# Performance work log

Measured on AMD Instinct MI355X. Metric: run time of the kernel, lower is better.

The kernel has to match this reference:

```python
import jax, jax.numpy as jnp
import numpy as np

D_MODEL = 2560
NUM_HEADS = 32
NUM_KV_HEADS = 8
HEAD_DIM = 128
ROPE_THETA = 5e6
EPS = 1e-6
G = NUM_KV_HEADS
Q_PER_KV = NUM_HEADS // NUM_KV_HEADS


def setup_inputs() -> dict:
    key = jax.random.key(0)
    ks = jax.random.split(key, 5)
    B, S = 1, 2048
    scale = 0.02
    return {
        "x": jax.random.normal(ks[0], (B, S, D_MODEL), jnp.float32),
        "Wq": jax.random.normal(ks[1], (NUM_HEADS * HEAD_DIM, D_MODEL), jnp.float32) * scale,
        "Wk": jax.random.normal(ks[2], (NUM_KV_HEADS * HEAD_DIM, D_MODEL), jnp.float32) * scale,
        "Wv": jax.random.normal(ks[3], (NUM_KV_HEADS * HEAD_DIM, D_MODEL), jnp.float32) * scale,
        "Wo": jax.random.normal(ks[4], (D_MODEL, NUM_HEADS * HEAD_DIM), jnp.float32) * scale,
        "q_norm_w": jnp.ones((HEAD_DIM,), jnp.float32),
        "k_norm_w": jnp.ones((HEAD_DIM,), jnp.float32),
    }


def _rms_norm(x, w):
    var = jnp.mean(jnp.square(x), axis=-1, keepdims=True)
    return x * jax.lax.rsqrt(var + EPS) * w


def _rope(x, pos):
    # x: (b, h, s, d); HF-style rotate_half RoPE
    d = x.shape[-1]
    inv_freq = 1.0 / (ROPE_THETA ** (jnp.arange(0, d, 2, dtype=jnp.float32) / d))
    ang = pos[:, None].astype(jnp.float32) * inv_freq[None, :]      # (s, d/2)
    cos = jnp.concatenate([jnp.cos(ang), jnp.cos(ang)], axis=-1)     # (s, d)
    sin = jnp.concatenate([jnp.sin(ang), jnp.sin(ang)], axis=-1)
    x1, x2 = x[..., : d // 2], x[..., d // 2 :]
    rot = jnp.concatenate([-x2, x1], axis=-1)
    return x * cos + rot * sin


def reference(x, Wq, Wk, Wv, Wo, q_norm_w, k_norm_w):
    B, S, _ = x.shape
    pos = jnp.arange(S)
    q = (x @ Wq.T).reshape(B, S, NUM_HEADS, HEAD_DIM).transpose(0, 2, 1, 3)
    k = (x @ Wk.T).reshape(B, S, NUM_KV_HEADS, HEAD_DIM).transpose(0, 2, 1, 3)
    v = (x @ Wv.T).reshape(B, S, NUM_KV_HEADS, HEAD_DIM).transpose(0, 2, 1, 3)
    q = _rope(_rms_norm(q, q_norm_w), pos)
    k = _rope(_rms_norm(k, k_norm_w), pos)
    new_cache_k, new_cache_v = k, v
    # GQA: (b, g, h, s, d) against (b, g, k, d)
    qg = q.reshape(B, G, Q_PER_KV, S, HEAD_DIM)
    scores = jnp.einsum("bghsd,bgkd->bghsk", qg, k) / (HEAD_DIM ** 0.5)
    causal = jnp.triu(jnp.full((S, S), -jnp.inf, jnp.float32), k=1)
    scores = scores + causal
    attn = jax.nn.softmax(scores, axis=-1)
    out = jnp.einsum("bghsk,bgkd->bghsd", attn, v)
    out = out.reshape(B, NUM_HEADS, S, HEAD_DIM).transpose(0, 2, 1, 3).reshape(B, S, NUM_HEADS * HEAD_DIM)
    out = out @ Wo.T
    return (out, new_cache_k, new_cache_v)
```

## Files before the change

### kernel.cpp

```cpp
#include <hip/hip_runtime.h>
#include <hip/hip_bf16.h>
#include <math.h>

#define S_LEN  2048
#define DMODEL 2560
#define NHEADS 32
#define NKV    8
#define HD     128
#define QKDIM  (NHEADS * HD)
#define KVDIM  (NKV * HD)

typedef __bf16 bf16x8 __attribute__((ext_vector_type(8)));
typedef float  f32x4  __attribute__((ext_vector_type(4)));
typedef unsigned short u16;

#define AS1 __attribute__((address_space(1)))
#define AS3 __attribute__((address_space(3)))

__device__ __forceinline__ void load16_to_lds(const void* g, void* l) {
    __builtin_amdgcn_global_load_lds((const AS1 void*)g, (AS3 void*)l, 16, 0, 0);
}

__device__ __forceinline__ u16 f2bf(float f) {
    unsigned u = __builtin_bit_cast(unsigned, f);
    return (u16)((u + 0x7fff + ((u >> 16) & 1)) >> 16);
}

#define PHASE_BAR() do { __builtin_amdgcn_sched_barrier(0);            \
                         __builtin_amdgcn_s_barrier();                 \
                         __builtin_amdgcn_sched_barrier(0); } while (0)
#define WAIT_LGKM0() do { asm volatile("s_waitcnt lgkmcnt(0)" ::: "memory"); \
                          __builtin_amdgcn_sched_barrier(0); } while (0)

__device__ __forceinline__ const bf16x8* fragp(const __bf16* hbase, int row, int colb) {
    int b = (row << 7) | colb;
    b ^= ((b >> 9) & 1) << 5;
    return (const bf16x8*)((const char*)hbase + b);
}

__device__ __forceinline__ void stage_half(const __bf16* __restrict__ g0, int Kp,
                                           __bf16* l0, int wave, int lane) {
#pragma unroll
    for (int j = 0; j < 2; ++j) {
        const int p = ((wave * 2 + j) << 10) | (lane << 4);
        const int b = p ^ (((p >> 9) & 1) << 5);
        load16_to_lds((const char*)g0 + (size_t)(b >> 7) * (Kp * 2) + (b & 127),
                      (char*)l0 + ((wave * 2 + j) << 10));
    }
}

#define N4_X   (S_LEN * DMODEL / 4)
#define N4_WQ  (QKDIM * DMODEL / 4)
#define N4_WK  (KVDIM * DMODEL / 4)
#define N4_ALL (N4_X + N4_WQ + 2 * N4_WK)

__global__ __launch_bounds__(256) void convert_inputs(const float* __restrict__ x,
                                                      const float* __restrict__ wq,
                                                      const float* __restrict__ wk,
                                                      const float* __restrict__ wv,
                                                      u16* __restrict__ xb,
                                                      u16* __restrict__ wb) {
    const int stride = gridDim.x * 256;
    for (int i = blockIdx.x * 256 + threadIdx.x; i < N4_ALL; i += stride) {
        const float4* src;
        ushort4* dst;
        if (i < N4_X) {
            src = (const float4*)x + i;
            dst = (ushort4*)xb + i;
        } else {
            const int j = i - N4_X;
            dst = (ushort4*)wb + j;
            if (j < N4_WQ)                  src = (const float4*)wq + j;
            else if (j < N4_WQ + N4_WK)     src = (const float4*)wk + (j - N4_WQ);
            else                            src = (const float4*)wv + (j - N4_WQ - N4_WK);
        }
        float4 v = *src;
        ushort4 r;
        r.x = f2bf(v.x); r.y = f2bf(v.y); r.z = f2bf(v.z); r.w = f2bf(v.w);
        *dst = r;
    }
}

__global__ __launch_bounds__(256) void f32_to_bf16_k(const float* __restrict__ in,
                                                     u16* __restrict__ out, int n4) {
    int i = blockIdx.x * 256 + threadIdx.x;
    const int stride = gridDim.x * 256;
    for (; i < n4; i += stride) {
        float4 v = ((const float4*)in)[i];
        ushort4 r;
        r.x = f2bf(v.x); r.y = f2bf(v.y); r.z = f2bf(v.z); r.w = f2bf(v.w);
        ((ushort4*)out)[i] = r;
    }
}

__global__ __launch_bounds__(64) void rope_table(float* __restrict__ ct,
                                                 float* __restrict__ st) {
    const int s = blockIdx.x;
    const int i = threadIdx.x;
    const double invf = pow(5.0e6, -(double)i / 64.0);
    const double ang  = (double)s * invf;
    ct[s * 64 + i] = (float)cos(ang);
    st[s * 64 + i] = (float)sin(ang);
}

__global__ __launch_bounds__(256) void gemm_bf16_nt(const __bf16* __restrict__ A,
                                                    const __bf16* __restrict__ B,
                                                    float* __restrict__ C,
                                                    int M, int N, int K) {
    __shared__ __align__(16) __bf16 Als[128 * 64];
    __shared__ __align__(16) __bf16 Bls[128 * 64];
    const int tid  = threadIdx.x;
    const int lane = tid & 63;
    const int wave = tid >> 6;
    const int wm   = wave >> 1, wn = wave & 1;
    const int m0   = blockIdx.y * 128;
    const int n0   = blockIdx.x * 128;
    const int frow = lane & 15;
    const int fkq  = lane >> 4;

    f32x4 acc[4][4];
#pragma unroll
    for (int t = 0; t < 4; ++t)
#pragma unroll
        for (int u = 0; u < 4; ++u)
            acc[t][u] = (f32x4){0.f, 0.f, 0.f, 0.f};

    for (int k0 = 0; k0 < K; k0 += 64) {
        __syncthreads();
#pragma unroll
        for (int i = 0; i < 2; ++i) {
            const int mt  = i * 4 + wave;
            const int row = mt * 16 + frow;
#pragma unroll
            for (int kh = 0; kh < 2; ++kh) {
                const int col = k0 + kh * 32 + fkq * 8;
                load16_to_lds(A + (size_t)(m0 + row) * K + col,
                              &Als[(size_t)((mt * 2 + kh) * 64) * 8]);
                load16_to_lds(B + (size_t)(n0 + row) * K + col,
                              &Bls[(size_t)((mt * 2 + kh) * 64) * 8]);
            }
        }
        __syncthreads();

#pragma unroll
        for (int kh = 0; kh < 2; ++kh) {
            bf16x8 af[4], bfr[4];
#pragma unroll
            for (int t = 0; t < 4; ++t)
                af[t]  = *(const bf16x8*)&Als[(((wm * 4 + t) * 2 + kh) * 64 + lane) * 8];
#pragma unroll
            for (int u = 0; u < 4; ++u)
                bfr[u] = *(const bf16x8*)&Bls[(((wn * 4 + u) * 2 + kh) * 64 + lane) * 8];
#pragma unroll
            for (int t = 0; t < 4; ++t)
#pragma unroll
                for (int u = 0; u < 4; ++u)
                    acc[t][u] = __builtin_amdgcn_mfma_f32_16x16x32_bf16(
                                    af[t], bfr[u], acc[t][u], 0, 0, 0);
        }
    }

    const int crow = (lane >> 4) * 4;
    const int ccol = lane & 15;
#pragma unroll
    for (int t = 0; t < 4; ++t) {
        const int gr = m0 + (wm * 4 + t) * 16 + crow;
#pragma unroll
        for (int u = 0; u < 4; ++u) {
            const int gc = n0 + (wn * 4 + u) * 16 + ccol;
#pragma unroll
            for (int r = 0; r < 4; ++r)
                C[(size_t)(gr + r) * N + gc] = acc[t][u][r];
        }
    }
}

__global__ __launch_bounds__(512, 2) void gemm_qkv_8ph(const __bf16* __restrict__ A,
                                                       const __bf16* __restrict__ Bq,
                                                       const __bf16* __restrict__ Bkv,
                                                       const float* __restrict__ ct,
                                                       const float* __restrict__ st,
                                                       const float* __restrict__ qw,
                                                       const float* __restrict__ kw,
                                                       u16*   __restrict__ qrb,
                                                       float* __restrict__ kc,
                                                       u16*   __restrict__ kcb,
                                                       float* __restrict__ vc,
                                                       u16*   __restrict__ vtb) {
    __shared__ __align__(16) __bf16 Als[4][128 * 64];
    __shared__ __align__(16) __bf16 Bls[4][128 * 64];

    const int K   = DMODEL;
    const int nkt = K / 64;
    const int n0g = blockIdx.x * 256;
    const __bf16* B;
    int n0;
    if (n0g < QKDIM) { B = Bq;  n0 = n0g; }
    else             { B = Bkv; n0 = n0g - QKDIM; }
    const int m0 = blockIdx.y * 256;

    const int tid  = threadIdx.x;
    const int lane = tid & 63;
    const int wave = tid >> 6;
    const int wm   = wave >> 1;
    const int wn   = wave & 1;
    const int frow = lane & 15;
    const int fkq  = lane >> 4;
    const int ha   = wm >> 1;
    const int ar0  = (wm & 1) * 64 + frow;

    f32x4 acc[4][8];
#pragma unroll
    for (int t = 0; t < 4; ++t)
#pragma unroll
        for (int u = 0; u < 8; ++u)
            acc[t][u] = (f32x4){0.f, 0.f, 0.f, 0.f};

    stage_half(A + (size_t)m0 * K,               K, Als[0], wave, lane);
    stage_half(A + (size_t)(m0 + 128) * K,       K, Als[1], wave, lane);
    stage_half(B + (size_t)n0 * K,               K, Bls[0], wave, lane);
    stage_half(B + (size_t)(n0 + 128) * K,       K, Bls[1], wave, lane);
    stage_half(A + (size_t)m0 * K + 64,          K, Als[2], wave, lane);
    stage_half(B + (size_t)n0 * K + 64,          K, Bls[2], wave, lane);
    stage_half(B + (size_t)(n0 + 128) * K + 64,  K, Bls[3], wave, lane);
    asm volatile("s_waitcnt vmcnt(6)" ::: "memory");
    PHASE_BAR();

    for (int kt = 0; kt < nkt; ++kt) {
        const int bf = kt & 1;
        const __bf16* Ahb = Als[bf * 2 + ha];
        const __bf16* Bhb = Bls[bf * 2 + wn];

        bf16x8 a0[2][2], b0[4][2];
#pragma unroll
        for (int mt = 0; mt < 2; ++mt)
#pragma unroll
            for (int kh = 0; kh < 2; ++kh)
                a0[mt][kh] = *fragp(Ahb, ar0 + mt * 16, kh * 64 + fkq * 16);
#pragma unroll
        for (int nt = 0; nt < 4; ++nt)
#pragma unroll
            for (int kh = 0; kh < 2; ++kh)
                b0[nt][kh] = *fragp(Bhb, nt * 16 + frow, kh * 64 + fkq * 16);
        if (kt + 1 < nkt)
            stage_half(A + (size_t)(m0 + 128) * K + (kt + 1) * 64, K,
                       Als[(bf ^ 1) * 2 + 1], wave, lane);
        asm volatile("s_waitcnt lgkmcnt(8)" ::: "memory");
        PHASE_BAR();
        WAIT_LGKM0();
        __builtin_amdgcn_s_setprio(1);
#pragma unroll
        for (int mt = 0; mt < 2; ++mt)
#pragma unroll
            for (int nt = 0; nt < 4; ++nt)
#pragma unroll
                for (int kh = 0; kh < 2; ++kh)
                    acc[mt][nt] = __builtin_amdgcn_mfma_f32_16x16x32_bf16(
                                      a0[mt][kh], b0[nt][kh], acc[mt][nt], 0, 0, 0);
        __builtin_amdgcn_s_setprio(0);
        PHASE_BAR();

        bf16x8 a1[2][2];
#pragma unroll
        for (int mt = 0; mt < 2; ++mt)
#pragma unroll
            for (int kh = 0; kh < 2; ++kh)
                a1[mt][kh] = *fragp(Ahb, ar0 + 32 + mt * 16, kh * 64 + fkq * 16);
        PHASE_BAR();
        WAIT_LGKM0();
        __builtin_amdgcn_s_setprio(1);
#pragma unroll
        for (int mt = 0; mt < 2; ++mt)
#pragma unroll
            for (int nt = 0; nt < 4; ++nt)
#pragma unroll
                for (int kh = 0; kh < 2; ++kh)
                    acc[2 + mt][nt] = __builtin_amdgcn_mfma_f32_16x16x32_bf16(
                                          a1[mt][kh], b0[nt][kh], acc[2 + mt][nt], 0, 0, 0);
        __builtin_amdgcn_s_setprio(0);
        PHASE_BAR();

        bf16x8 b1[4][2];
#pragma unroll
        for (int nt = 0; nt < 4; ++nt)
#pragma unroll
            for (int kh = 0; kh < 2; ++kh)
                b1[nt][kh] = *fragp(Bhb, (4 + nt) * 16 + frow, kh * 64 + fkq * 16);
        if (kt + 2 < nkt)
            stage_half(A + (size_t)m0 * K + (kt + 2) * 64, K,
                       Als[bf * 2 + 0], wave, lane);
        PHASE_BAR();
        WAIT_LGKM0();
        __builtin_amdgcn_s_setprio(1);
#pragma unroll
        for (int mt = 0; mt < 2; ++mt)
#pragma unroll
            for (int nt = 0; nt < 4; ++nt)
#pragma unroll
                for (int kh = 0; kh < 2; ++kh)
                    acc[2 + mt][4 + nt] = __builtin_amdgcn_mfma_f32_16x16x32_bf16(
                                              a1[mt][kh], b1[nt][kh], acc[2 + mt][4 + nt], 0, 0, 0);
        __builtin_amdgcn_s_setprio(0);
        PHASE_BAR();

        if (kt + 2 < nkt) {
            stage_half(B + (size_t)n0 * K + (kt + 2) * 64,         K,
                       Bls[bf * 2 + 0], wave, lane);
            stage_half(B + (size_t)(n0 + 128) * K + (kt + 2) * 64, K,
                       Bls[bf * 2 + 1], wave, lane);
        }
        PHASE_BAR();
        WAIT_LGKM0();
        __builtin_amdgcn_s_setprio(1);
#pragma unroll
        for (int mt = 0; mt < 2; ++mt)
#pragma unroll
            for (int nt = 0; nt < 4; ++nt)
#pragma unroll
                for (int kh = 0; kh < 2; ++kh)
                    acc[mt][4 + nt] = __builtin_amdgcn_mfma_f32_16x16x32_bf16(
                                          a0[mt][kh], b1[nt][kh], acc[mt][4 + nt], 0, 0, 0);
        __builtin_amdgcn_s_setprio(0);
        if (kt < nkt - 2) asm volatile("s_waitcnt vmcnt(6)" ::: "memory");
        else              asm volatile("s_waitcnt vmcnt(0)" ::: "memory");
        PHASE_BAR();
    }

    const int fr = frow;
    const int fq = fkq;
    const int nw = n0g + wn * 128;
    if (n0g < QKDIM + KVDIM) {
        const int isQ = (n0g < QKDIM) ? 1 : 0;
        const float* w = isQ ? qw : kw;
        float wv[8];
#pragma unroll
        for (int u = 0; u < 8; ++u) wv[u] = w[u * 16 + fr];

#pragma unroll
        for (int mt = 0; mt < 4; ++mt) {
#pragma unroll
            for (int r = 0; r < 4; ++r) {
                float ss = 0.f;
#pragma unroll
                for (int u = 0; u < 8; ++u) ss += acc[mt][u][r] * acc[mt][u][r];
                ss += __shfl_xor(ss, 1);
                ss += __shfl_xor(ss, 2);
                ss += __shfl_xor(ss, 4);
                ss += __shfl_xor(ss, 8);
                const float rstd = rsqrtf(ss * (1.0f / 128.0f) + 1e-6f);
                const int s = m0 + wm * 64 + mt * 16 + fq * 4 + r;
#pragma unroll
                for (int u = 0; u < 4; ++u) {
                    const float cs  = ct[s * 64 + u * 16 + fr];
                    const float sn  = st[s * 64 + u * 16 + fr];
                    const float ylo = acc[mt][u][r]     * rstd * wv[u];
                    const float yhi = acc[mt][u + 4][r] * rstd * wv[u + 4];
                    const float olo = ylo * cs - yhi * sn;
                    const float ohi = yhi * cs + ylo * sn;
                    if (isQ) {
                        const int h = nw >> 7;
                        const size_t base = ((size_t)h * S_LEN + s) * HD;
                        qrb[base + u * 16 + fr]       = f2bf(olo * 0.12751743f);
                        qrb[base + (u + 4) * 16 + fr] = f2bf(ohi * 0.12751743f);
                    } else {
                        const int g = (nw - QKDIM) >> 7;
                        const size_t base = ((size_t)g * S_LEN + s) * HD;
                        kc [base + u * 16 + fr]       = olo;
                        kc [base + (u + 4) * 16 + fr] = ohi;
                        kcb[base + u * 16 + fr]       = f2bf(olo);
                        kcb[base + (u + 4) * 16 + fr] = f2bf(ohi);
                    }
                }
            }
        }
    } else {
        const int g = (nw - QKDIM - KVDIM) >> 7;
#pragma unroll
        for (int mt = 0; mt < 4; ++mt) {
            const int sb = m0 + wm * 64 + mt * 16 + fq * 4;
#pragma unroll
            for (int u = 0; u < 8; ++u) {
                const int d = u * 16 + fr;
                ushort4 o;
                o.x = f2bf(acc[mt][u][0]); o.y = f2bf(acc[mt][u][1]);
                o.z = f2bf(acc[mt][u][2]); o.w = f2bf(acc[mt][u][3]);
                *(ushort4*)&vtb[((size_t)g * HD + d) * S_LEN + sb] = o;
#pragma unroll
                for (int r = 0; r < 4; ++r)
                    vc[((size_t)g * S_LEN + sb + r) * HD + d] = acc[mt][u][r];
            }
        }
    }
}

__device__ __forceinline__ void attn_tile_compute(
        const bf16x8 aq[4], f32x4 o_acc[8], float m_i[4], float l_i[4],
        const __bf16* __restrict__ Kl, const __bf16* __restrict__ Vl,
        __bf16* __restrict__ Pls, int lane, int wave, int fr, int fq,
        int qrow0, int kbase, bool diag) {
    f32x4 s_acc[4];
#pragma unroll
    for (int u = 0; u < 4; ++u) s_acc[u] = (f32x4){0.f, 0.f, 0.f, 0.f};
    __builtin_amdgcn_s_setprio(1);
#pragma unroll
    for (int u = 0; u < 4; ++u)
#pragma unroll
        for (int ks = 0; ks < 4; ++ks)
            s_acc[u] = __builtin_amdgcn_mfma_f32_16x16x32_bf16(
                           aq[ks],
                           *(const bf16x8*)&Kl[((u * 4 + ks) * 64 + lane) * 8],
                           s_acc[u], 0, 0, 0);
    __builtin_amdgcn_s_setprio(0);

    if (diag) {
#pragma unroll
        for (int u = 0; u < 4; ++u)
#pragma unroll
            for (int r = 0; r < 4; ++r)
                if (kbase + u * 16 + fr > qrow0 + fq * 4 + r)
                    s_acc[u][r] = -INFINITY;
    }

#pragma unroll
    for (int r = 0; r < 4; ++r) {
        float mx = fmaxf(fmaxf(s_acc[0][r], s_acc[1][r]),
                         fmaxf(s_acc[2][r], s_acc[3][r]));
#pragma unroll
        for (int off = 1; off < 16; off <<= 1)
            mx = fmaxf(mx, __shfl_xor(mx, off));
        const float m_new = fmaxf(m_i[r], mx);
        const float alpha = exp2f(m_i[r] - m_new);
        m_i[r] = m_new;

        float p[4], psum = 0.0f;
#pragma unroll
        for (int u = 0; u < 4; ++u) {
            p[u] = exp2f(s_acc[u][r] - m_new);
            psum += p[u];
        }
#pragma unroll
        for (int off = 1; off < 16; off <<= 1)
            psum += __shfl_xor(psum, off);
        l_i[r] = l_i[r] * alpha + psum;

#pragma unroll
        for (int dt = 0; dt < 8; ++dt) o_acc[dt][r] *= alpha;

#pragma unroll
        for (int u = 0; u < 4; ++u) {
            const int k = u * 16 + fr;
            const int m = fq * 4 + r;
            const int idx = ((wave * 2 + (k >> 5)) * 64 + ((k >> 3) & 3) * 16 + m) * 8
                            + (k & 7);
            ((u16*)Pls)[idx] = f2bf(p[u]);
        }
    }

    bf16x8 ap[2];
#pragma unroll
    for (int ks = 0; ks < 2; ++ks)
        ap[ks] = *(const bf16x8*)&Pls[((wave * 2 + ks) * 64 + lane) * 8];
    __builtin_amdgcn_s_setprio(1);
#pragma unroll
    for (int dt = 0; dt < 8; ++dt)
#pragma unroll
        for (int ks = 0; ks < 2; ++ks)
            o_acc[dt] = __builtin_amdgcn_mfma_f32_16x16x32_bf16(
                            ap[ks],
                            *(const bf16x8*)&Vl[((dt * 2 + ks) * 64 + lane) * 8],
                            o_acc[dt], 0, 0, 0);
    __builtin_amdgcn_s_setprio(0);
}

__global__ __launch_bounds__(256) void attn_mfma(const __bf16* __restrict__ Qb,
                                                 const __bf16* __restrict__ Kb,
                                                 const __bf16* __restrict__ Vt,
                                                 u16* __restrict__ Ob) {
    __shared__ __align__(16) __bf16 Kls[2][16 * 64 * 8];
    __shared__ __align__(16) __bf16 Vls[2][16 * 64 * 8];
    __shared__ __align__(16) __bf16 Pls[8 * 64 * 8];

    const int h    = blockIdx.x;
    const int g    = h >> 2;
    const int pair = blockIdx.y;
    const int ytl  = pair;
    const int yth  = (S_LEN / 64 - 1) - pair;
    const int q0l  = ytl * 64;
    const int q0h  = yth * 64;
    const int tid  = threadIdx.x;
    const int lane = tid & 63;
    const int wave = tid >> 6;
    const int fr   = lane & 15;
    const int fq   = lane >> 4;

    {
        const __bf16* Qh = Qb + ((size_t)h * S_LEN + q0h + wave * 16 + fr) * HD;
        const __bf16* Ql = Qb + ((size_t)h * S_LEN + q0l + wave * 16 + fr) * HD;
#pragma unroll
        for (int ks = 0; ks < 4; ++ks) {
            load16_to_lds(Qh + ks * 32 + fq * 8, &Kls[0][(size_t)((wave * 4 + ks) * 64) * 8]);
            load16_to_lds(Ql + ks * 32 + fq * 8, &Kls[1][(size_t)((wave * 4 + ks) * 64) * 8]);
        }
    }
    __syncthreads();
    bf16x8 aqh[4], aql[4];
#pragma unroll
    for (int ks = 0; ks < 4; ++ks) {
        aqh[ks] = *(const bf16x8*)&Kls[0][((wave * 4 + ks) * 64 + lane) * 8];
        aql[ks] = *(const bf16x8*)&Kls[1][((wave * 4 + ks) * 64 + lane) * 8];
    }
    __syncthreads();

    float m_h[4], l_h[4], m_l[4], l_l[4];
    f32x4 o_h[8], o_l[8];
#pragma unroll
    for (int r = 0; r < 4; ++r) {
        m_h[r] = -INFINITY; l_h[r] = 0.0f;
        m_l[r] = -INFINITY; l_l[r] = 0.0f;
    }
#pragma unroll
    for (int dt = 0; dt < 8; ++dt) {
        o_h[dt] = (f32x4){0.f, 0.f, 0.f, 0.f};
        o_l[dt] = (f32x4){0.f, 0.f, 0.f, 0.f};
    }

    {
        const __bf16* Kg = Kb + ((size_t)g * S_LEN + wave * 16 + fr) * HD;
#pragma unroll
        for (int ks = 0; ks < 4; ++ks)
            load16_to_lds(Kg + ks * 32 + fq * 8, &Kls[0][(size_t)((wave * 4 + ks) * 64) * 8]);
#pragma unroll
        for (int i = 0; i < 2; ++i) {
            const int dt = wave * 2 + i;
            const __bf16* Vg = Vt + ((size_t)g * HD + dt * 16 + fr) * S_LEN;
#pragma unroll
            for (int ks = 0; ks < 2; ++ks)
                load16_to_lds(Vg + ks * 32 + fq * 8, &Vls[0][(size_t)((dt * 2 + ks) * 64) * 8]);
        }
    }
    __syncthreads();

    for (int kt = 0; kt <= yth; ++kt) {
        const int buf = kt & 1;
        if (kt < yth) {
            const int nb = buf ^ 1;
            const __bf16* Kg = Kb + ((size_t)g * S_LEN + (kt + 1) * 64 + wave * 16 + fr) * HD;
#pragma unroll
            for (int ks = 0; ks < 4; ++ks)
                load16_to_lds(Kg + ks * 32 + fq * 8, &Kls[nb][(size_t)((wave * 4 + ks) * 64) * 8]);
#pragma unroll
            for (int i = 0; i < 2; ++i) {
                const int dt = wave * 2 + i;
                const __bf16* Vg = Vt + ((size_t)g * HD + dt * 16 + fr) * S_LEN + (kt + 1) * 64;
#pragma unroll
                for (int ks = 0; ks < 2; ++ks)
                    load16_to_lds(Vg + ks * 32 + fq * 8, &Vls[nb][(size_t)((dt * 2 + ks) * 64) * 8]);
            }
        }

        attn_tile_compute(aqh, o_h, m_h, l_h, Kls[buf], Vls[buf], Pls,
                          lane, wave, fr, fq, q0h + wave * 16, kt * 64, kt == yth);
        if (kt <= ytl)
            attn_tile_compute(aql, o_l, m_l, l_l, Kls[buf], Vls[buf], Pls,
                              lane, wave, fr, fq, q0l + wave * 16, kt * 64, kt == ytl);

        __syncthreads();
    }

#pragma unroll
    for (int r = 0; r < 4; ++r) {
        const float ih = 1.0f / l_h[r];
        const float il = 1.0f / l_l[r];
        const int sh = q0h + wave * 16 + fq * 4 + r;
        const int sl = q0l + wave * 16 + fq * 4 + r;
#pragma unroll
        for (int dt = 0; dt < 8; ++dt) {
            Ob[(size_t)sh * QKDIM + h * HD + dt * 16 + fr] = f2bf(o_h[dt][r] * ih);
            Ob[(size_t)sl * QKDIM + h * HD + dt * 16 + fr] = f2bf(o_l[dt][r] * il);
        }
    }
}

extern "C" void kernel_launch(void* const* d_in, const int* in_sizes, int n_in,
                              void* d_out, int out_size, void* d_ws, size_t ws_size,
                              hipStream_t stream) {
    const float* x  = (const float*)d_in[0];
    const float* Wq = (const float*)d_in[1];
    const float* Wk = (const float*)d_in[2];
    const float* Wv = (const float*)d_in[3];
    const float* Wo = (const float*)d_in[4];
    const float* qw = (const float*)d_in[5];
    const float* kw = (const float*)d_in[6];

    float* out     = (float*)d_out;
    float* cache_k = out + (size_t)S_LEN * DMODEL;
    float* cache_v = cache_k + (size_t)NKV * S_LEN * HD;

    u16* wsu = (u16*)d_ws;
    u16* qrb = wsu;
    u16* kcb = qrb + (size_t)NHEADS * S_LEN * HD;
    u16* vtb = kcb + (size_t)NKV * S_LEN * HD;
    u16* Wqb = vtb + (size_t)NKV * S_LEN * HD;
    u16* Wkb = Wqb + (size_t)QKDIM * DMODEL;
    u16* aob = Wqb;
    u16* Wob = aob + (size_t)S_LEN * QKDIM;
    float* ct = (float*)(Wqb + (size_t)S_LEN * QKDIM + (size_t)DMODEL * QKDIM);
    float* st = ct + S_LEN * 64;
    u16* xb  = (u16*)out;

    convert_inputs<<<4096, 256, 0, stream>>>(x, Wq, Wk, Wv, xb, Wqb);
    rope_table<<<S_LEN, 64, 0, stream>>>(ct, st);

    gemm_qkv_8ph<<<dim3((QKDIM + 2 * KVDIM) / 256, S_LEN / 256), 512, 0, stream>>>(
        (const __bf16*)xb, (const __bf16*)Wqb, (const __bf16*)Wkb,
        ct, st, qw, kw, qrb, cache_k, kcb, cache_v, vtb);

    f32_to_bf16_k<<<1024, 256, 0, stream>>>(Wo, Wob, DMODEL * QKDIM / 4);
    attn_mfma<<<dim3(NHEADS, S_LEN / 128), 256, 0, stream>>>(
        (const __bf16*)qrb, (const __bf16*)kcb, (const __bf16*)vtb, aob);

    gemm_bf16_nt<<<dim3(DMODEL / 128, S_LEN / 128), 256, 0, stream>>>(
        (const __bf16*)aob, (const __bf16*)Wob, out, S_LEN, DMODEL, QKDIM);
}
```

Baseline: 484.9 us.

## Compute transposed attention scores, lazily rescale softmax, pass P through registers

The attention inner tile now computes S^T (K as the A operand), so each lane holds one query column. Row max and sum then need only two cross-lane shuffles instead of 16-wide butterflies per row. The online-softmax rescale is skipped unless the max grows by more than a threshold, and P is packed to bf16 with v_cvt_pk and moved into the PV operand layout by shuffles, which removes the LDS round trip for P. Separately, the GEMM LDS swizzle is changed to a 3-bit XOR and the attention kernel gets a launch-bounds occupancy hint of 2, trading added shuffle work and register pressure for fewer LDS accesses and bank conflicts.

```diff
diff --git a/kernel.cpp b/kernel.cpp
--- a/kernel.cpp
+++ b/kernel.cpp
@@ -34,7 +34,7 @@
 
 __device__ __forceinline__ const bf16x8* fragp(const __bf16* hbase, int row, int colb) {
     int b = (row << 7) | colb;
-    b ^= ((b >> 9) & 1) << 5;
+    b ^= ((b >> 7) & 7) << 4;
     return (const bf16x8*)((const char*)hbase + b);
 }
 
@@ -43,7 +43,7 @@
 #pragma unroll
     for (int j = 0; j < 2; ++j) {
         const int p = ((wave * 2 + j) << 10) | (lane << 4);
-        const int b = p ^ (((p >> 9) & 1) << 5);
+        const int b = p ^ (((p >> 7) & 7) << 4);
         load16_to_lds((const char*)g0 + (size_t)(b >> 7) * (Kp * 2) + (b & 127),
                       (char*)l0 + ((wave * 2 + j) << 10));
     }
@@ -393,23 +393,21 @@
     }
 }
 
-__device__ __forceinline__ void attn_tile_compute(
-        const bf16x8 aq[4], f32x4 o_acc[8], float m_i[4], float l_i[4],
+__device__ __forceinline__ void attn_tile_swapped(
+        const bf16x8 aq[4], f32x4 o_acc[8], float& m_i, float& l_i,
         const __bf16* __restrict__ Kl, const __bf16* __restrict__ Vl,
-        __bf16* __restrict__ Pls, int lane, int wave, int fr, int fq,
-        int qrow0, int kbase, bool diag) {
-    f32x4 s_acc[4];
-#pragma unroll
-    for (int u = 0; u < 4; ++u) s_acc[u] = (f32x4){0.f, 0.f, 0.f, 0.f};
+        int lane, int fr, int fq, int qm, int kbase, bool diag) {
+    f32x4 sT[4];
+#pragma unroll
+    for (int u = 0; u < 4; ++u) sT[u] = (f32x4){0.f, 0.f, 0.f, 0.f};
     __builtin_amdgcn_s_setprio(1);
 #pragma unroll
     for (int u = 0; u < 4; ++u)
 #pragma unroll
         for (int ks = 0; ks < 4; ++ks)
-            s_acc[u] = __builtin_amdgcn_mfma_f32_16x16x32_bf16(
-                           aq[ks],
-                           *(const bf16x8*)&Kl[((u * 4 + ks) * 64 + lane) * 8],
-                           s_acc[u], 0, 0, 0);
+            sT[u] = __builtin_amdgcn_mfma_f32_16x16x32_bf16(
+                        *(const bf16x8*)&Kl[((u * 4 + ks) * 64 + lane) * 8],
+                        aq[ks], sT[u], 0, 0, 0);
     __builtin_amdgcn_s_setprio(0);
 
     if (diag) {
@@ -417,49 +415,68 @@
         for (int u = 0; u < 4; ++u)
 #pragma unroll
             for (int r = 0; r < 4; ++r)
-                if (kbase + u * 16 + fr > qrow0 + fq * 4 + r)
-                    s_acc[u][r] = -INFINITY;
-    }
-
-#pragma unroll
-    for (int r = 0; r < 4; ++r) {
-        float mx = fmaxf(fmaxf(s_acc[0][r], s_acc[1][r]),
-                         fmaxf(s_acc[2][r], s_acc[3][r]));
-#pragma unroll
-        for (int off = 1; off < 16; off <<= 1)
-            mx = fmaxf(mx, __shfl_xor(mx, off));
-        const float m_new = fmaxf(m_i[r], mx);
-        const float alpha = exp2f(m_i[r] - m_new);
-        m_i[r] = m_new;
-
-        float p[4], psum = 0.0f;
-#pragma unroll
-        for (int u = 0; u < 4; ++u) {
-            p[u] = exp2f(s_acc[u][r] - m_new);
-            psum += p[u];
-        }
-#pragma unroll
-        for (int off = 1; off < 16; off <<= 1)
-            psum += __shfl_xor(psum, off);
-        l_i[r] = l_i[r] * alpha + psum;
-
-#pragma unroll
-        for (int dt = 0; dt < 8; ++dt) o_acc[dt][r] *= alpha;
-
-#pragma unroll
-        for (int u = 0; u < 4; ++u) {
-            const int k = u * 16 + fr;
-            const int m = fq * 4 + r;
-            const int idx = ((wave * 2 + (k >> 5)) * 64 + ((k >> 3) & 3) * 16 + m) * 8
-                            + (k & 7);
-            ((u16*)Pls)[idx] = f2bf(p[u]);
-        }
-    }
-
+                if (kbase + u * 16 + fq * 4 + r > qm + fr)
+                    sT[u][r] = -INFINITY;
+    }
+
+    float mx = sT[0][0];
+#pragma unroll
+    for (int u = 0; u < 4; ++u)
+#pragma unroll
+        for (int r = 0; r < 4; ++r) mx = fmaxf(mx, sT[u][r]);
+    mx = fmaxf(mx, __shfl_xor(mx, 16));
+    mx = fmaxf(mx, __shfl_xor(mx, 32));
+
+    if (__any(mx > m_i + 8.0f)) {
+        const float m_new = fmaxf(m_i, mx);
+        const float alpha = exp2f(m_i - m_new);
+        m_i = m_new;
+        l_i *= alpha;
+#pragma unroll
+        for (int r = 0; r < 4; ++r) {
+            const float a = __shfl(alpha, fq * 4 + r);
+#pragma unroll
+            for (int dt = 0; dt < 8; ++dt) o_acc[dt][r] *= a;
+        }
+    }
+
+    float p[4][4];
+    float ps = 0.f;
+#pragma unroll
+    for (int u = 0; u < 4; ++u)
+#pragma unroll
+        for (int r = 0; r < 4; ++r) {
+            p[u][r] = exp2f(sT[u][r] - m_i);
+            ps += p[u][r];
+        }
+    ps += __shfl_xor(ps, 16);
+    ps += __shfl_xor(ps, 32);
+    l_i += ps;
+
+    unsigned pk[4][2];
+#pragma unroll
+    for (int u = 0; u < 4; ++u)
+#pragma unroll
+        for (int hh = 0; hh < 2; ++hh)
+            asm("v_cvt_pk_bf16_f32 %0, %1, %2"
+                : "=v"(pk[u][hh]) : "v"(p[u][2 * hh]), "v"(p[u][2 * hh + 1]));
+
+    const int slA = fr + 16 * ((fq & 1) * 2);
+    const int slB = slA + 16;
     bf16x8 ap[2];
 #pragma unroll
-    for (int ks = 0; ks < 2; ++ks)
-        ap[ks] = *(const bf16x8*)&Pls[((wave * 2 + ks) * 64 + lane) * 8];
+    for (int ks = 0; ks < 2; ++ks) {
+        unsigned w[4];
+#pragma unroll
+        for (int jp = 0; jp < 4; ++jp) {
+            const int sl = (jp & 2) ? slB : slA;
+            const unsigned v0 = (unsigned)__shfl((int)pk[2 * ks + 0][jp & 1], sl);
+            const unsigned v1 = (unsigned)__shfl((int)pk[2 * ks + 1][jp & 1], sl);
+            w[jp] = (fq & 2) ? v1 : v0;
+        }
+        ap[ks] = __builtin_bit_cast(bf16x8, (uint4){w[0], w[1], w[2], w[3]});
+    }
+
     __builtin_amdgcn_s_setprio(1);
 #pragma unroll
     for (int dt = 0; dt < 8; ++dt)
@@ -472,13 +489,12 @@
     __builtin_amdgcn_s_setprio(0);
 }
 
-__global__ __launch_bounds__(256) void attn_mfma(const __bf16* __restrict__ Qb,
-                                                 const __bf16* __restrict__ Kb,
-                                                 const __bf16* __restrict__ Vt,
-                                                 u16* __restrict__ Ob) {
+__global__ __launch_bounds__(256, 2) void attn_mfma(const __bf16* __restrict__ Qb,
+                                                    const __bf16* __restrict__ Kb,
+                                                    const __bf16* __restrict__ Vt,
+                                                    u16* __restrict__ Ob) {
     __shared__ __align__(16) __bf16 Kls[2][16 * 64 * 8];
     __shared__ __align__(16) __bf16 Vls[2][16 * 64 * 8];
-    __shared__ __align__(16) __bf16 Pls[8 * 64 * 8];
 
     const int h    = blockIdx.x;
     const int g    = h >> 2;
@@ -511,13 +527,8 @@
     }
     __syncthreads();
 
-    float m_h[4], l_h[4], m_l[4], l_l[4];
+    float m_h = -INFINITY, l_h = 0.f, m_l = -INFINITY, l_l = 0.f;
     f32x4 o_h[8], o_l[8];
-#pragma unroll
-    for (int r = 0; r < 4; ++r) {
-        m_h[r] = -INFINITY; l_h[r] = 0.0f;
-        m_l[r] = -INFINITY; l_l[r] = 0.0f;
-    }
 #pragma unroll
     for (int dt = 0; dt < 8; ++dt) {
         o_h[dt] = (f32x4){0.f, 0.f, 0.f, 0.f};
@@ -558,19 +569,19 @@
             }
         }
 
-        attn_tile_compute(aqh, o_h, m_h, l_h, Kls[buf], Vls[buf], Pls,
-                          lane, wave, fr, fq, q0h + wave * 16, kt * 64, kt == yth);
+        attn_tile_swapped(aqh, o_h, m_h, l_h, Kls[buf], Vls[buf],
+                          lane, fr, fq, q0h + wave * 16, kt * 64, kt == yth);
         if (kt <= ytl)
-            attn_tile_compute(aql, o_l, m_l, l_l, Kls[buf], Vls[buf], Pls,
-                              lane, wave, fr, fq, q0l + wave * 16, kt * 64, kt == ytl);
+            attn_tile_swapped(aql, o_l, m_l, l_l, Kls[buf], Vls[buf],
+                              lane, fr, fq, q0l + wave * 16, kt * 64, kt == ytl);
 
         __syncthreads();
     }
 
 #pragma unroll
     for (int r = 0; r < 4; ++r) {
-        const float ih = 1.0f / l_h[r];
-        const float il = 1.0f / l_l[r];
+        const float ih = 1.0f / __shfl(l_h, fq * 4 + r);
+        const float il = 1.0f / __shfl(l_l, fq * 4 + r);
         const int sh = q0h + wave * 16 + fq * 4 + r;
         const int sl = q0l + wave * 16 + fq * 4 + r;
 #pragma unroll
```

Result: faster. 455.0 us (-6.2%).
